# Performance work log

Hardware: AMD Instinct MI355X
Metric: run time of the kernel (lower is better)

Reference implementation:

```python
import jax, jax.numpy as jnp
import numpy as np

N_NODES = 50000
N_EDGES = 800000
IN_CH = 128
HEADS = 4
OUT_CH = 32
NEG_SLOPE = 0.2


def setup_inputs() -> dict:
    key = jax.random.key(0)
    ks = jax.random.split(key, 8)
    x = jax.random.normal(ks[0], (N_NODES, IN_CH), dtype=jnp.float32)
    # edges guaranteed to have no self-loops (module removes then re-adds them)
    tgt = jax.random.randint(ks[1], (N_EDGES,), 0, N_NODES)
    off = jax.random.randint(ks[2], (N_EDGES,), 1, N_NODES)
    src = (tgt + off) % N_NODES
    edge_index = jnp.stack([src, tgt]).astype(jnp.int64)
    glorot = lambda k, shp: jax.random.uniform(
        k, shp, jnp.float32, -1.0, 1.0) * np.sqrt(6.0 / (shp[-1] + shp[-2]))
    Wl = glorot(ks[3], (HEADS * OUT_CH, IN_CH))  # torch Linear weight [out,in]
    Wr = glorot(ks[4], (HEADS * OUT_CH, IN_CH))
    att = glorot(ks[5], (1, HEADS, OUT_CH))
    bl = jnp.zeros((HEADS * OUT_CH,), jnp.float32)
    br = jnp.zeros((HEADS * OUT_CH,), jnp.float32)
    bias = jnp.zeros((HEADS * OUT_CH,), jnp.float32)
    return {"x": x, "edge_index": edge_index, "Wl": Wl, "bl": bl,
            "Wr": Wr, "br": br, "att": att, "bias": bias}


def _forward(x, edge_index, Wl, bl, Wr, br, att, bias):
    H, C = HEADS, OUT_CH
    n = x.shape[0]
    x_l = (x @ Wl.T + bl).reshape(n, H, C)  # target projection
    x_r = (x @ Wr.T + br).reshape(n, H, C)  # source projection
    # add self-loops (inputs contain none by construction)
    loops = jnp.arange(n, dtype=edge_index.dtype)
    src = jnp.concatenate([edge_index[0], loops])
    tgt = jnp.concatenate([edge_index[1], loops])
    x_i = x_l[tgt]                     # [E', H, C]
    x_j = x_r[src]                     # [E', H, C]
    a_in = jax.nn.leaky_relu(x_i + x_j, NEG_SLOPE)
    alpha = jnp.einsum('ehc,ohc->eh', a_in, att)  # [E', H]
    # segment softmax over target nodes
    m = jax.ops.segment_max(alpha, tgt, num_segments=n)
    alpha = jnp.exp(alpha - jax.lax.stop_gradient(m)[tgt])
    denom = jax.ops.segment_sum(alpha, tgt, num_segments=n)
    alpha = alpha / denom[tgt]
    msgs = x_j * alpha[:, :, None]     # [E', H, C]
    out = jax.ops.segment_sum(msgs, tgt, num_segments=n)  # [N, H, C]
    out = out.reshape(n, H * C) + bias  # concat=True
    return out


def reference(x, edge_index, Wl, bl, Wr, br, att, bias):
    return _forward(x, edge_index, Wl, bl, Wr, br, att, bias)
```

## Files before the change

kernel.cpp:

```cpp
#include <hip/hip_runtime.h>
#include <hip/hip_bf16.h>
#include <stdint.h>

#define N_NODES 50000
#define N_EDGES 800000
#define IN_CH   128
#define NEG_SLOPE 0.2f

#define NBUCK   196
#define E1      4000
#define FILLB   200
#define BCAP    6144
#define BSTRIDE 24576
#define CAPR    48

#define E_PER 8
#define FILL_BLOCKS 391

typedef short short8 __attribute__((ext_vector_type(8)));
typedef float f32x4  __attribute__((ext_vector_type(4)));
typedef float f32x2  __attribute__((ext_vector_type(2)));

static __device__ __forceinline__ float bf_lo(uint32_t p) { return __uint_as_float(p << 16); }
static __device__ __forceinline__ float bf_hi(uint32_t p) { return __uint_as_float(p & 0xffff0000u); }
static __device__ __forceinline__ uint16_t f_to_bf(float f) {
    uint32_t u = __float_as_uint(f);
    u += 0x7fffu + ((u >> 16) & 1u);
    return (uint16_t)(u >> 16);
}

static __device__ __forceinline__ f32x2 lrelu2(f32x2 x) {
    f32x2 s = x * NEG_SLOPE;
    f32x2 r;
    r[0] = fmaxf(x[0], s[0]);
    r[1] = fmaxf(x[1], s[1]);
    return r;
}

static __device__ __forceinline__ float sum16(float x) {
    x += __uint_as_float(__builtin_amdgcn_update_dpp(0, __float_as_uint(x), 0xB1,  0xf, 0xf, true));
    x += __uint_as_float(__builtin_amdgcn_update_dpp(0, __float_as_uint(x), 0x4E,  0xf, 0xf, true));
    x += __uint_as_float(__builtin_amdgcn_update_dpp(0, __float_as_uint(x), 0x141, 0xf, 0xf, true));
    x += __uint_as_float(__builtin_amdgcn_update_dpp(0, __float_as_uint(x), 0x140, 0xf, 0xf, true));
    return x;
}

static __device__ __forceinline__ void sum16x2(float& a, float& b) {
    asm("s_nop 0\n\t"
        "v_add_f32 %0, %0, %0 quad_perm:[1,0,3,2] row_mask:0xf bank_mask:0xf bound_ctrl:0\n\t"
        "v_add_f32 %1, %1, %1 quad_perm:[1,0,3,2] row_mask:0xf bank_mask:0xf bound_ctrl:0\n\t"
        "v_add_f32 %0, %0, %0 quad_perm:[2,3,0,1] row_mask:0xf bank_mask:0xf bound_ctrl:0\n\t"
        "v_add_f32 %1, %1, %1 quad_perm:[2,3,0,1] row_mask:0xf bank_mask:0xf bound_ctrl:0\n\t"
        "v_add_f32 %0, %0, %0 row_half_mirror row_mask:0xf bank_mask:0xf bound_ctrl:0\n\t"
        "v_add_f32 %1, %1, %1 row_half_mirror row_mask:0xf bank_mask:0xf bound_ctrl:0\n\t"
        "v_add_f32 %0, %0, %0 row_mirror row_mask:0xf bank_mask:0xf bound_ctrl:0\n\t"
        "v_add_f32 %1, %1, %1 row_mirror row_mask:0xf bank_mask:0xf bound_ctrl:0"
        : "+v"(a), "+v"(b));
}

static __device__ __forceinline__ void wswz_body(
    int t, const float* __restrict__ Wl, const float* __restrict__ Wr,
    __hip_bfloat16* __restrict__ wswz)
{
    int ct = t >> 8, rem = t & 255;
    int ch = rem >> 6, lane = rem & 63;
    int m = lane & 15, quad = lane >> 4;
    const float* W = (ct < 8) ? Wl : Wr;
    int o = ((ct & 7) << 4) + m;
    const float* src = W + (size_t)o * IN_CH + ch * 32 + quad * 8;
    short8 f;
#pragma unroll
    for (int j = 0; j < 8; ++j) f[j] = (short)f_to_bf(src[j]);
    *(short8*)((short*)wswz + (size_t)t * 8) = f;
}

static __device__ __forceinline__ void proj_body(
    int rowbase, int tid,
    const float* __restrict__ x, const __hip_bfloat16* __restrict__ wswz,
    const float* __restrict__ bl, const float* __restrict__ br,
    float* __restrict__ xl, __hip_bfloat16* __restrict__ xr)
{
    int lane = tid & 63;
    int widx = tid >> 6;
    int m = lane & 15;
    int quad = lane >> 4;

    short8 afrag[4];
    const float* xrow = x + (size_t)(rowbase + m) * IN_CH;
#pragma unroll
    for (int ch = 0; ch < 4; ++ch) {
        f32x4 p0 = *(const f32x4*)(xrow + ch * 32 + quad * 8);
        f32x4 p1 = *(const f32x4*)(xrow + ch * 32 + quad * 8 + 4);
        short8 f;
#pragma unroll
        for (int j = 0; j < 4; ++j) { f[j] = (short)f_to_bf(p0[j]); f[j + 4] = (short)f_to_bf(p1[j]); }
        afrag[ch] = f;
    }

    const short* wz = (const short*)wswz;
    const float* bv = (widx < 2) ? bl : br;
#pragma unroll
    for (int cc = 0; cc < 4; ++cc) {
        int ct = widx * 4 + cc;
        int o = ((ct & 7) << 4) + m;
        f32x4 acc = {0.f, 0.f, 0.f, 0.f};
#pragma unroll
        for (int ch = 0; ch < 4; ++ch) {
            short8 bfrag = *(const short8*)(wz + ((size_t)(ct * 4 + ch) * 64 + lane) * 8);
            acc = __builtin_amdgcn_mfma_f32_16x16x32_bf16(afrag[ch], bfrag, acc, 0, 0, 0);
        }
        float bias_v = bv[o];
        if (widx < 2) {
#pragma unroll
            for (int r = 0; r < 4; ++r)
                xl[(size_t)(rowbase + quad * 4 + r) * IN_CH + o] = acc[r] + bias_v;
        } else {
#pragma unroll
            for (int r = 0; r < 4; ++r)
                xr[(size_t)(rowbase + quad * 4 + r) * IN_CH + o] = __float2bfloat16(acc[r] + bias_v);
        }
    }
}

__global__ __launch_bounds__(256) void prep_kernel(
    const float* __restrict__ Wl, const float* __restrict__ Wr,
    __hip_bfloat16* __restrict__ wswz, int* __restrict__ z, int zn)
{
    int t = blockIdx.x * 256 + threadIdx.x;
    if (t < 4096) wswz_body(t, Wl, Wr, wswz);
    for (int i = t; i < zn; i += 64 * 256) z[i] = 0;
}

__global__ __launch_bounds__(256) void proj_fill(
    const float* __restrict__ x, const __hip_bfloat16* __restrict__ wswz,
    const float* __restrict__ bl, const float* __restrict__ br,
    float* __restrict__ xl, __hip_bfloat16* __restrict__ xr,
    const int* __restrict__ ei, uint32_t* __restrict__ bcnt,
    char* __restrict__ region)
{
    __shared__ uint32_t s_sorted[E1];
    __shared__ uint32_t s_hist[NBUCK], s_lstart[NBUCK], s_loc[NBUCK], s_gbase[NBUCK];
    __shared__ uint32_t s_T;

    if (blockIdx.x >= FILLB) {
        proj_body((blockIdx.x - FILLB) * 16, threadIdx.x, x, wswz, bl, br, xl, xr);
        return;
    }

    int tid = threadIdx.x;
    int fb = blockIdx.x;
    for (int i = tid; i < NBUCK; i += 256) s_hist[i] = 0;
    __syncthreads();

    const uint32_t* eiw = (const uint32_t*)ei;
    bool zlo = (eiw[2 * (tid & 63) + 1] == 0u);
    bool is64 = __popcll(__ballot(zlo)) >= 32;
    int e0 = fb * E1;

    for (int k = tid; k < E1; k += 256) {
        int e = e0 + k;
        int s = is64 ? (int)eiw[2 * (size_t)e] : ei[e];
        int t = is64 ? (int)eiw[2 * ((size_t)N_EDGES + e)] : ei[N_EDGES + e];
        if ((unsigned)s < N_NODES && (unsigned)t < N_NODES)
            atomicAdd(&s_hist[t >> 8], 1u);
    }
    __syncthreads();

    if (tid < NBUCK) s_gbase[tid] = atomicAdd(&bcnt[tid], s_hist[tid]);
    if (tid == 0) {
        uint32_t acc = 0;
        for (int i = 0; i < NBUCK; ++i) { s_lstart[i] = acc; acc += s_hist[i]; }
        s_T = acc;
    }
    __syncthreads();
    if (tid < NBUCK) s_loc[tid] = s_lstart[tid];
    __syncthreads();

    for (int k = tid; k < E1; k += 256) {
        int e = e0 + k;
        int s = is64 ? (int)eiw[2 * (size_t)e] : ei[e];
        int t = is64 ? (int)eiw[2 * ((size_t)N_EDGES + e)] : ei[N_EDGES + e];
        if ((unsigned)s < N_NODES && (unsigned)t < N_NODES) {
            uint32_t r = atomicAdd(&s_loc[t >> 8], 1u);
            s_sorted[r] = ((uint32_t)t << 16) | (uint32_t)s;
        }
    }
    __syncthreads();

    int T = (int)s_T;
    for (int k = tid; k < T; k += 256) {
        uint32_t v = s_sorted[k];
        uint32_t key = v >> 24;
        uint32_t g = s_gbase[key] + (uint32_t)k - s_lstart[key];
        if (g < BCAP)
            ((uint32_t*)(region + (size_t)key * BSTRIDE))[g] = v;
    }
}

__global__ __launch_bounds__(256) void csr_build(
    const uint32_t* __restrict__ bcnt, char* __restrict__ region,
    uint32_t* __restrict__ degs32)
{
    __shared__ uint16_t slab[256 * CAPR];
    __shared__ uint32_t lcnt[256];
    int b = blockIdx.x, tid = threadIdx.x;
    lcnt[tid] = 0;
    __syncthreads();

    uint32_t* reg = (uint32_t*)(region + (size_t)b * BSTRIDE);
    int M = min((int)bcnt[b], BCAP);
    for (int k = tid; k < M; k += 256) {
        uint32_t v = reg[k];
        int node = (int)((v >> 16) & 255u);
        uint32_t pos = atomicAdd(&lcnt[node], 1u);
        if (pos < CAPR) slab[node * CAPR + pos] = (uint16_t)(v & 0xffffu);
    }
    __syncthreads();

    const uint32_t* sw = (const uint32_t*)slab;
    for (int j = tid; j < (256 * CAPR / 2); j += 256) reg[j] = sw[j];
    if (tid < 64) {
        uint32_t p = 0;
#pragma unroll
        for (int q = 0; q < 4; ++q) {
            uint32_t d = min(lcnt[tid * 4 + q], (uint32_t)CAPR);
            p |= d << (q * 8);
        }
        degs32[b * 64 + tid] = p;
    }
}

__global__ __launch_bounds__(256) void fill_kernel(
    const int* __restrict__ ei, int cap,
    int* __restrict__ cnt, uint16_t* __restrict__ csr)
{
    const uint32_t* eiw = (const uint32_t*)ei;
    bool z = (eiw[2 * (threadIdx.x & 63) + 1] == 0u);
    bool is64 = __popcll(__ballot(z)) >= 32;

    int tid = blockIdx.x * 256 + threadIdx.x;
    int e0 = tid * E_PER;
    if (e0 >= N_EDGES) return;

    int src[E_PER], tgt[E_PER];
    if (is64) {
        const int4* ps = (const int4*)(eiw + 2 * (size_t)e0);
        const int4* pt = (const int4*)(eiw + 2 * ((size_t)N_EDGES + e0));
#pragma unroll
        for (int k = 0; k < 4; ++k) {
            int4 s = ps[k], t = pt[k];
            src[2 * k] = s.x; src[2 * k + 1] = s.z;
            tgt[2 * k] = t.x; tgt[2 * k + 1] = t.z;
        }
    } else {
        const int4* ps = (const int4*)(ei + e0);
        const int4* pt = (const int4*)(ei + N_EDGES + e0);
#pragma unroll
        for (int k = 0; k < 2; ++k) {
            int4 s = ps[k], t = pt[k];
            src[4 * k] = s.x; src[4 * k + 1] = s.y; src[4 * k + 2] = s.z; src[4 * k + 3] = s.w;
            tgt[4 * k] = t.x; tgt[4 * k + 1] = t.y; tgt[4 * k + 2] = t.z; tgt[4 * k + 3] = t.w;
        }
    }

    int pos[E_PER];
#pragma unroll
    for (int k = 0; k < E_PER; ++k) {
        bool ok = (unsigned)src[k] < N_NODES && (unsigned)tgt[k] < N_NODES;
        pos[k] = ok ? atomicAdd(&cnt[tgt[k]], 1) : cap;
    }
#pragma unroll
    for (int k = 0; k < E_PER; ++k)
        if (pos[k] < cap) csr[(size_t)tgt[k] * cap + pos[k]] = (uint16_t)src[k];
}

__global__ __launch_bounds__(256) void proj_kernel(
    const float* __restrict__ x, const __hip_bfloat16* __restrict__ wswz,
    const float* __restrict__ bl, const float* __restrict__ br,
    float* __restrict__ xl, __hip_bfloat16* __restrict__ xr)
{
    proj_body(blockIdx.x * 16, threadIdx.x, x, wswz, bl, br, xl, xr);
}

__global__ __launch_bounds__(256) void agg_kernel(
    const __hip_bfloat16* __restrict__ xr,
    const char* __restrict__ degbase, int degpacked,
    const uint16_t* __restrict__ csr, int ldcsr, int cap,
    const float* __restrict__ att, const float* __restrict__ bias,
    float* out )
{
    int n = blockIdx.x * 4 + (threadIdx.x >> 6);
    if (n >= N_NODES) return;
    int lane = threadIdx.x & 63;

    const uint32_t* xrw = (const uint32_t*)xr;

    f32x2 qv = *(const f32x2*)(out + (size_t)n * IN_CH + 2 * lane);
    f32x2 av = *(const f32x2*)(att + 2 * lane);
    av = av * 1.44269504088896f;
    f32x2 bv = *(const f32x2*)(bias + 2 * lane);

    int deg;
    if (degpacked) {
        uint32_t pk = ((const uint32_t*)degbase)[n >> 2];
        deg = (int)((pk >> ((n & 3) * 8)) & 255u);
    } else {
        deg = ((const int*)degbase)[n];
    }
    deg = min(deg, cap);

    const uint16_t* lst = csr + (size_t)n * ldcsr;
    int idxreg = (int)lst[min(lane, cap - 1)];

    uint32_t u = xrw[(size_t)n * 64 + lane];
    f32x2 a0v; a0v[0] = bf_lo(u); a0v[1] = bf_hi(u);
    f32x2 p0 = lrelu2(qv + a0v) * av;
    float t = sum16(p0[0] + p0[1]);
    float w = __builtin_amdgcn_exp2f(t);
    float lsum = w;
    f32x2 acc = w * a0v;

    if (deg > 0) {
        int dm1 = deg - 1;
        int sA0 = __builtin_amdgcn_readlane(idxreg, 0);
        int sB0 = __builtin_amdgcn_readlane(idxreg, min(1, dm1));
        int sA1 = __builtin_amdgcn_readlane(idxreg, min(2, dm1));
        int sB1 = __builtin_amdgcn_readlane(idxreg, min(3, dm1));
        int sA2 = __builtin_amdgcn_readlane(idxreg, min(4, dm1));
        int sB2 = __builtin_amdgcn_readlane(idxreg, min(5, dm1));
        uint32_t uA0 = xrw[(size_t)sA0 * 64 + lane];
        uint32_t uB0 = xrw[(size_t)sB0 * 64 + lane];
        uint32_t uA1 = xrw[(size_t)sA1 * 64 + lane];
        uint32_t uB1 = xrw[(size_t)sB1 * 64 + lane];
        uint32_t uA2 = xrw[(size_t)sA2 * 64 + lane];
        uint32_t uB2 = xrw[(size_t)sB2 * 64 + lane];
        int i = 0;
        while (i + 1 < deg) {
            int sA3 = __builtin_amdgcn_readlane(idxreg, min(i + 6, dm1));
            int sB3 = __builtin_amdgcn_readlane(idxreg, min(i + 7, dm1));
            uint32_t uA3 = xrw[(size_t)sA3 * 64 + lane];
            uint32_t uB3 = xrw[(size_t)sB3 * 64 + lane];

            f32x2 aA; aA[0] = bf_lo(uA0); aA[1] = bf_hi(uA0);
            f32x2 aB; aB[0] = bf_lo(uB0); aB[1] = bf_hi(uB0);
            f32x2 pA = lrelu2(qv + aA) * av;
            f32x2 pB = lrelu2(qv + aB) * av;
            float tA = pA[0] + pA[1];
            float tB = pB[0] + pB[1];
            sum16x2(tA, tB);
            float wA = __builtin_amdgcn_exp2f(tA), wB = __builtin_amdgcn_exp2f(tB);
            lsum += wA + wB;
            acc += wA * aA;
            acc += wB * aB;

            uA0 = uA1; uB0 = uB1;
            uA1 = uA2; uB1 = uB2;
            uA2 = uA3; uB2 = uB3;
            i += 2;
        }
        if (i < deg) {
            f32x2 aA; aA[0] = bf_lo(uA0); aA[1] = bf_hi(uA0);
            f32x2 pA = lrelu2(qv + aA) * av;
            float tA = sum16(pA[0] + pA[1]);
            float wA = __builtin_amdgcn_exp2f(tA);
            lsum += wA;
            acc += wA * aA;
        }
    }

    float inv = 1.f / lsum;
    f32x2 ov = acc * inv + bv;
    *(f32x2*)(out + (size_t)n * IN_CH + 2 * lane) = ov;
}

extern "C" void kernel_launch(void* const* d_in, const int* in_sizes, int n_in,
                              void* d_out, int out_size, void* d_ws, size_t ws_size,
                              hipStream_t stream) {
    const float* x    = (const float*)d_in[0];
    const int*   ei   = (const int*)d_in[1];
    const float* Wl   = (const float*)d_in[2];
    const float* bl   = (const float*)d_in[3];
    const float* Wr   = (const float*)d_in[4];
    const float* br   = (const float*)d_in[5];
    const float* att  = (const float*)d_in[6];
    const float* bias = (const float*)d_in[7];
    float* out = (float*)d_out;

    char* ws = (char*)d_ws;
    __hip_bfloat16* xr   = (__hip_bfloat16*)(ws);
    __hip_bfloat16* wswz = (__hip_bfloat16*)(ws + 12800000);

    const size_t DEGS_OFF = 12865536;
    const size_t BCNT_OFF = 12915712;
    const size_t REG_OFF  = 12916736;
    const size_t NEED     = REG_OFF + (size_t)NBUCK * BSTRIDE;

    if (ws_size >= NEED) {
        uint32_t* degs   = (uint32_t*)(ws + DEGS_OFF);
        uint32_t* bcnt   = (uint32_t*)(ws + BCNT_OFF);
        char*     region = ws + REG_OFF;

        prep_kernel<<<64, 256, 0, stream>>>(Wl, Wr, wswz, (int*)bcnt, NBUCK);
        proj_fill<<<FILLB + N_NODES / 16, 256, 0, stream>>>(
            x, wswz, bl, br, out, xr, ei, bcnt, region);
        csr_build<<<NBUCK, 256, 0, stream>>>(bcnt, region, degs);
        agg_kernel<<<N_NODES / 4, 256, 0, stream>>>(
            xr, (const char*)degs, 1, (const uint16_t*)region, CAPR, CAPR,
            att, bias, out);
    } else {
        const size_t CSR_BASE = 13065536;
        int*      cnt = (int*)(ws + 12865536);
        uint16_t* csr = (uint16_t*)(ws + CSR_BASE);
        long long avail = (ws_size > CSR_BASE) ? (long long)(ws_size - CSR_BASE) : 0;
        int cap = (int)(avail / ((long long)N_NODES * 2));
        if (cap > 64) cap = 64;
        if (cap < 1)  cap = 1;

        prep_kernel<<<64, 256, 0, stream>>>(Wl, Wr, wswz, cnt, N_NODES);
        fill_kernel<<<FILL_BLOCKS, 256, 0, stream>>>(ei, cap, cnt, csr);
        proj_kernel<<<N_NODES / 16, 256, 0, stream>>>(x, wswz, bl, br, out, xr);
        agg_kernel<<<N_NODES / 4, 256, 0, stream>>>(
            xr, (const char*)cnt, 0, csr, cap, cap, att, bias, out);
    }
}
```

Baseline: 164.5 us.

## Process two edges per wavefront in aggregation using half-wave splits

```diff
diff --git a/kernel.cpp b/kernel.cpp
--- a/kernel.cpp
+++ b/kernel.cpp
@@ -37,26 +37,7 @@
     return r;
 }
 
-static __device__ __forceinline__ float sum16(float x) {
-    x += __uint_as_float(__builtin_amdgcn_update_dpp(0, __float_as_uint(x), 0xB1,  0xf, 0xf, true));
-    x += __uint_as_float(__builtin_amdgcn_update_dpp(0, __float_as_uint(x), 0x4E,  0xf, 0xf, true));
-    x += __uint_as_float(__builtin_amdgcn_update_dpp(0, __float_as_uint(x), 0x141, 0xf, 0xf, true));
-    x += __uint_as_float(__builtin_amdgcn_update_dpp(0, __float_as_uint(x), 0x140, 0xf, 0xf, true));
-    return x;
-}
-
-static __device__ __forceinline__ void sum16x2(float& a, float& b) {
-    asm("s_nop 0\n\t"
-        "v_add_f32 %0, %0, %0 quad_perm:[1,0,3,2] row_mask:0xf bank_mask:0xf bound_ctrl:0\n\t"
-        "v_add_f32 %1, %1, %1 quad_perm:[1,0,3,2] row_mask:0xf bank_mask:0xf bound_ctrl:0\n\t"
-        "v_add_f32 %0, %0, %0 quad_perm:[2,3,0,1] row_mask:0xf bank_mask:0xf bound_ctrl:0\n\t"
-        "v_add_f32 %1, %1, %1 quad_perm:[2,3,0,1] row_mask:0xf bank_mask:0xf bound_ctrl:0\n\t"
-        "v_add_f32 %0, %0, %0 row_half_mirror row_mask:0xf bank_mask:0xf bound_ctrl:0\n\t"
-        "v_add_f32 %1, %1, %1 row_half_mirror row_mask:0xf bank_mask:0xf bound_ctrl:0\n\t"
-        "v_add_f32 %0, %0, %0 row_mirror row_mask:0xf bank_mask:0xf bound_ctrl:0\n\t"
-        "v_add_f32 %1, %1, %1 row_mirror row_mask:0xf bank_mask:0xf bound_ctrl:0"
-        : "+v"(a), "+v"(b));
-}
+#define DPPADD(x, ctrl) __uint_as_float(__builtin_amdgcn_update_dpp(0, __float_as_uint(x), ctrl, 0xf, 0xf, true))
 
 static __device__ __forceinline__ void wswz_body(
     int t, const float* __restrict__ Wl, const float* __restrict__ Wr,
@@ -292,13 +273,19 @@
     int n = blockIdx.x * 4 + (threadIdx.x >> 6);
     if (n >= N_NODES) return;
     int lane = threadIdx.x & 63;
-
-    const uint32_t* xrw = (const uint32_t*)xr;
-
-    f32x2 qv = *(const f32x2*)(out + (size_t)n * IN_CH + 2 * lane);
-    f32x2 av = *(const f32x2*)(att + 2 * lane);
-    av = av * 1.44269504088896f;
-    f32x2 bv = *(const f32x2*)(bias + 2 * lane);
+    int lpos = lane & 31;
+    bool isB = lane >= 32;
+
+    const char* xrb = (const char*)xr;
+
+    f32x4 qv4 = *(const f32x4*)(out + (size_t)n * IN_CH + lpos * 4);
+    f32x4 av4 = *(const f32x4*)(att + lpos * 4);
+    f32x4 bv4 = *(const f32x4*)(bias + lpos * 4);
+    f32x2 q01; q01[0] = qv4[0]; q01[1] = qv4[1];
+    f32x2 q23; q23[0] = qv4[2]; q23[1] = qv4[3];
+    const float L2E = 1.44269504088896f;
+    f32x2 a01; a01[0] = av4[0] * L2E; a01[1] = av4[1] * L2E;
+    f32x2 a23; a23[0] = av4[2] * L2E; a23[1] = av4[3] * L2E;
 
     int deg;
     if (degpacked) {
@@ -308,69 +295,73 @@
         deg = ((const int*)degbase)[n];
     }
     deg = min(deg, cap);
+    deg = min(deg, 63);
 
     const uint16_t* lst = csr + (size_t)n * ldcsr;
-    int idxreg = (int)lst[min(lane, cap - 1)];
-
-    uint32_t u = xrw[(size_t)n * 64 + lane];
-    f32x2 a0v; a0v[0] = bf_lo(u); a0v[1] = bf_hi(u);
-    f32x2 p0 = lrelu2(qv + a0v) * av;
-    float t = sum16(p0[0] + p0[1]);
-    float w = __builtin_amdgcn_exp2f(t);
-    float lsum = w;
-    f32x2 acc = w * a0v;
-
-    if (deg > 0) {
-        int dm1 = deg - 1;
-        int sA0 = __builtin_amdgcn_readlane(idxreg, 0);
-        int sB0 = __builtin_amdgcn_readlane(idxreg, min(1, dm1));
-        int sA1 = __builtin_amdgcn_readlane(idxreg, min(2, dm1));
-        int sB1 = __builtin_amdgcn_readlane(idxreg, min(3, dm1));
-        int sA2 = __builtin_amdgcn_readlane(idxreg, min(4, dm1));
-        int sB2 = __builtin_amdgcn_readlane(idxreg, min(5, dm1));
-        uint32_t uA0 = xrw[(size_t)sA0 * 64 + lane];
-        uint32_t uB0 = xrw[(size_t)sB0 * 64 + lane];
-        uint32_t uA1 = xrw[(size_t)sA1 * 64 + lane];
-        uint32_t uB1 = xrw[(size_t)sB1 * 64 + lane];
-        uint32_t uA2 = xrw[(size_t)sA2 * 64 + lane];
-        uint32_t uB2 = xrw[(size_t)sB2 * 64 + lane];
-        int i = 0;
-        while (i + 1 < deg) {
-            int sA3 = __builtin_amdgcn_readlane(idxreg, min(i + 6, dm1));
-            int sB3 = __builtin_amdgcn_readlane(idxreg, min(i + 7, dm1));
-            uint32_t uA3 = xrw[(size_t)sA3 * 64 + lane];
-            uint32_t uB3 = xrw[(size_t)sB3 * 64 + lane];
-
-            f32x2 aA; aA[0] = bf_lo(uA0); aA[1] = bf_hi(uA0);
-            f32x2 aB; aB[0] = bf_lo(uB0); aB[1] = bf_hi(uB0);
-            f32x2 pA = lrelu2(qv + aA) * av;
-            f32x2 pB = lrelu2(qv + aB) * av;
-            float tA = pA[0] + pA[1];
-            float tB = pB[0] + pB[1];
-            sum16x2(tA, tB);
-            float wA = __builtin_amdgcn_exp2f(tA), wB = __builtin_amdgcn_exp2f(tB);
-            lsum += wA + wB;
-            acc += wA * aA;
-            acc += wB * aB;
-
-            uA0 = uA1; uB0 = uB1;
-            uA1 = uA2; uB1 = uB2;
-            uA2 = uA3; uB2 = uB3;
-            i += 2;
-        }
-        if (i < deg) {
-            f32x2 aA; aA[0] = bf_lo(uA0); aA[1] = bf_hi(uA0);
-            f32x2 pA = lrelu2(qv + aA) * av;
-            float tA = sum16(pA[0] + pA[1]);
-            float wA = __builtin_amdgcn_exp2f(tA);
-            lsum += wA;
-            acc += wA * aA;
-        }
-    }
+    int idxreg = (int)lst[min(max(lane - 1, 0), cap - 1)];
+    idxreg = (lane == 0) ? n : idxreg;
+
+    int last = deg;
+    int FP   = (deg + 1) >> 1;
+    int ODD  = (deg + 1) & 1;
+
+    float lsum = 0.f;
+    f32x2 acc0 = {0.f, 0.f}, acc1 = {0.f, 0.f};
+
+#define PAIR_LOAD(p, udst) { \
+        int sa_ = __builtin_amdgcn_readlane(idxreg, min(2 * (p), last)); \
+        int sb_ = __builtin_amdgcn_readlane(idxreg, min(2 * (p) + 1, last)); \
+        int vs_ = isB ? sb_ : sa_; \
+        udst = *(const uint2*)(xrb + (uint32_t)vs_ * 256u + (uint32_t)lpos * 8u); \
+    }
+
+#define PAIR_EVAL(u, MASKED) { \
+        f32x2 c0_, c1_; \
+        c0_[0] = bf_lo((u).x); c0_[1] = bf_hi((u).x); \
+        c1_[0] = bf_lo((u).y); c1_[1] = bf_hi((u).y); \
+        f32x2 r0_ = lrelu2(q01 + c0_) * a01; \
+        f32x2 r1_ = lrelu2(q23 + c1_) * a23; \
+        float t_ = (r0_[0] + r0_[1]) + (r1_[0] + r1_[1]); \
+        t_ += DPPADD(t_, 0xB1);    \
+        t_ += DPPADD(t_, 0x4E);    \
+        t_ += DPPADD(t_, 0x141);   \
+        float w_ = __builtin_amdgcn_exp2f(t_); \
+        if (MASKED) w_ = isB ? 0.f : w_; \
+        lsum += w_; \
+        acc0 += w_ * c0_; \
+        acc1 += w_ * c1_; \
+    }
+
+    uint2 u0, u1;
+    PAIR_LOAD(0, u0);
+    PAIR_LOAD(1, u1);
+    for (int p = 0; p < FP; ++p) {
+        uint2 u2;
+        PAIR_LOAD(p + 2, u2);
+        PAIR_EVAL(u0, false);
+        u0 = u1; u1 = u2;
+    }
+    if (ODD) {
+        PAIR_EVAL(u0, true);
+    }
+
+    lsum    += __shfl_xor(lsum,    32);
+    acc0[0] += __shfl_xor(acc0[0], 32);
+    acc0[1] += __shfl_xor(acc0[1], 32);
+    acc1[0] += __shfl_xor(acc1[0], 32);
+    acc1[1] += __shfl_xor(acc1[1], 32);
 
     float inv = 1.f / lsum;
-    f32x2 ov = acc * inv + bv;
-    *(f32x2*)(out + (size_t)n * IN_CH + 2 * lane) = ov;
+    if (lane < 32) {
+        f32x4 ov;
+        ov[0] = acc0[0] * inv + bv4[0];
+        ov[1] = acc0[1] * inv + bv4[1];
+        ov[2] = acc1[0] * inv + bv4[2];
+        ov[3] = acc1[1] * inv + bv4[3];
+        *(f32x4*)(out + (size_t)n * IN_CH + lpos * 4) = ov;
+    }
+#undef PAIR_LOAD
+#undef PAIR_EVAL
 }
 
 extern "C" void kernel_launch(void* const* d_in, const int* in_sizes, int n_in,
```

New measurement: 162.3 us. Within noise of the previous version (-1.3%).
